# Optimization experiments

Measured on AMD Instinct MI355X. Metric: run time of the kernel, lower is better.

## Reference

```python
import jax, jax.numpy as jnp
import numpy as np

N_NODES = 50000
N_EDGES = 800000
D_FEAT = 64      # node feature dim -> edge input is 2*D_FEAT
HIDDEN = 128     # ebm hidden width (== 2*D_FEAT here)


def setup_inputs() -> dict:
    key = jax.random.key(0)
    ks = jax.random.split(key, 8)
    x = jax.random.normal(ks[0], (N_NODES, D_FEAT), dtype=jnp.float32)
    edge_index = jax.random.randint(ks[1], (2, N_EDGES), 0, N_NODES, dtype=jnp.int64)
    t = jax.random.uniform(ks[2], (N_EDGES,), dtype=jnp.float32)
    s1 = 1.0 / np.sqrt(2 * D_FEAT)
    s2 = 1.0 / np.sqrt(HIDDEN)
    W1 = jax.random.normal(ks[3], (2 * D_FEAT, HIDDEN), dtype=jnp.float32) * s1
    b1 = jnp.zeros((HIDDEN,), dtype=jnp.float32)
    Wt = jax.random.normal(ks[4], (1, HIDDEN), dtype=jnp.float32)
    bt = jnp.zeros((HIDDEN,), dtype=jnp.float32)
    W2 = jax.random.normal(ks[5], (HIDDEN, 2 * D_FEAT), dtype=jnp.float32) * s2
    b2 = jnp.zeros((2 * D_FEAT,), dtype=jnp.float32)
    return {"x": x, "edge_index": edge_index, "t": t,
            "W1": W1, "b1": b1, "Wt": Wt, "bt": bt, "W2": W2, "b2": b2}


def _ebm(edge_input, t, W1, b1, Wt, bt, W2, b2):
    # time-conditioned 2-layer SiLU MLP: [E, 2d] -> [E, 2d]
    t_emb = jax.nn.silu(t[:, None] * Wt + bt)            # [E, H]
    h = jax.nn.silu(edge_input @ W1 + t_emb + b1)        # [E, H]
    return h @ W2 + b2                                    # [E, 2d]


def reference(x, edge_index, t, W1, b1, Wt, bt, W2, b2):
    row, col = edge_index[0], edge_index[1]
    # gather endpoint features and concat -> [E, 2d]
    edge_input = jnp.concatenate([x[row], x[col]], axis=1)
    edge_output = _ebm(edge_input, t, W1, b1, Wt, bt, W2, b2)
    d = edge_output.shape[1] // 2
    src_update = edge_output[:, :d]
    tgt_update = edge_output[:, d:]
    update = jnp.concatenate([src_update, tgt_update], axis=0)  # [2E, d]
    idx = jnp.concatenate([row, col], axis=0)                   # [2E]
    # scatter_add into node slots
    return jax.ops.segment_sum(update, idx, num_segments=x.shape[0])
```

## Files before the change

kernel.cpp:

```cpp
#include <hip/hip_runtime.h>
#include <hip/hip_bf16.h>

#define NEDGE 800000
#define NNODE 50000
#define DF    64
#define HID   128
#define NTILE (NEDGE / 16)
#define BLK   768
#define WPB   12
#define TBINS 2048

using short8 = __attribute__((ext_vector_type(8))) short;
using f32x4  = __attribute__((ext_vector_type(4))) float;
using i32x4  = __attribute__((ext_vector_type(4))) int;

union P8 { unsigned int u[4]; short8 s; };

__device__ __forceinline__ unsigned int pk2(float lo, float hi) {
    union { __hip_bfloat162 p; unsigned int u; } c;
    c.p = __float22bfloat162_rn(float2{lo, hi});
    return c.u;
}

__device__ __forceinline__ unsigned short bf1(float f) {
    union { __hip_bfloat16 b; unsigned short u; } c;
    c.b = __float2bfloat16(f);
    return c.u;
}

__device__ __forceinline__ float bf2f(unsigned short u) {
    union { unsigned int i; float f; } c;
    c.i = ((unsigned int)u) << 16;
    return c.f;
}

__device__ __forceinline__ float exp2_hw(float x) {
    float r; asm("v_exp_f32 %0, %1" : "=v"(r) : "v"(x)); return r;
}
__device__ __forceinline__ float rcp_hw(float x) {
    float r; asm("v_rcp_f32 %0, %1" : "=v"(r) : "v"(x)); return r;
}
__device__ __forceinline__ float silu_f(float v) {
    return v * rcp_hw(1.0f + exp2_hw(v * -1.44269504f));
}

__device__ __forceinline__ short8 te_load(const unsigned short* __restrict__ ttbl,
                                          float tv, int jl) {
    const int tb = (int)(tv * (float)TBINS);
    return *(const short8*)(ttbl + (size_t)tb * HID + (jl << 3));
}

__device__ __forceinline__ int swz(int r, int k) {
    return (r << 8) + ((((k >> 3) ^ (r & 7)) << 4) | ((k & 7) << 1));
}
__device__ __forceinline__ int swz16(int r, int slot) {
    return (r << 8) + ((slot ^ (r & 7)) << 4);
}

__global__ void __launch_bounds__(256)
prep_kernel(const float* __restrict__ x, unsigned short* __restrict__ xb,
            const float* __restrict__ Wt, const float* __restrict__ bt,
            unsigned short* __restrict__ ttbl, int* __restrict__ counts)
{
    const int i = blockIdx.x * 256 + threadIdx.x;
    if (i < NNODE * DF / 8) {
        const f32x4 u = *(const f32x4*)(x + (size_t)i * 8);
        const f32x4 v = *(const f32x4*)(x + (size_t)i * 8 + 4);
        P8 p;
        p.u[0] = pk2(u[0], u[1]); p.u[1] = pk2(u[2], u[3]);
        p.u[2] = pk2(v[0], v[1]); p.u[3] = pk2(v[2], v[3]);
        *(short8*)(xb + (size_t)i * 8) = p.s;
    }
    if (i < TBINS * HID / 8) {
        const int bin = i >> 4;
        const int j0  = (i & 15) << 3;
        const float tv = (bin + 0.5f) * (1.0f / (float)TBINS);
        float e[8];
#pragma unroll
        for (int q = 0; q < 8; q++) e[q] = silu_f(fmaf(tv, Wt[j0 + q], bt[j0 + q]));
        P8 p;
        p.u[0] = pk2(e[0], e[1]); p.u[1] = pk2(e[2], e[3]);
        p.u[2] = pk2(e[4], e[5]); p.u[3] = pk2(e[6], e[7]);
        *(short8*)(ttbl + (size_t)bin * HID + j0) = p.s;
    }
    if (i < NNODE) counts[i] = 0;
}

__global__ void __launch_bounds__(256) hist_kernel(const int* __restrict__ ei,
                                                   int* __restrict__ counts) {
    const int i = blockIdx.x * 256 + threadIdx.x;
    if (i < 2 * NEDGE) atomicAdd(&counts[ei[i]], 1);
}

__global__ void __launch_bounds__(1024) scan1_kernel(const int* __restrict__ counts,
                                                     int* __restrict__ offs,
                                                     int* __restrict__ bsum) {
    __shared__ int buf[1024];
    const int tid = threadIdx.x;
    const int gid = blockIdx.x * 1024 + tid;
    const int v = (gid < NNODE) ? counts[gid] : 0;
    buf[tid] = v;
    __syncthreads();
#pragma unroll
    for (int off = 1; off < 1024; off <<= 1) {
        const int u = (tid >= off) ? buf[tid - off] : 0;
        __syncthreads();
        buf[tid] += u;
        __syncthreads();
    }
    if (gid < NNODE) offs[gid] = buf[tid] - v;
    if (tid == 1023) bsum[blockIdx.x] = buf[1023];
}

__global__ void __launch_bounds__(1024) scan2_kernel(int* __restrict__ bsum, int nb) {
    __shared__ int buf[1024];
    const int tid = threadIdx.x;
    const int v = (tid < nb) ? bsum[tid] : 0;
    buf[tid] = v;
    __syncthreads();
#pragma unroll
    for (int off = 1; off < 1024; off <<= 1) {
        const int u = (tid >= off) ? buf[tid - off] : 0;
        __syncthreads();
        buf[tid] += u;
        __syncthreads();
    }
    if (tid < nb) bsum[tid] = buf[tid] - v;
}

__global__ void __launch_bounds__(1024) scan3_kernel(int* __restrict__ offs,
                                                     const int* __restrict__ bsum,
                                                     int* __restrict__ cursor) {
    const int gid = blockIdx.x * 1024 + threadIdx.x;
    if (gid < NNODE) {
        const int o = offs[gid] + bsum[blockIdx.x];
        offs[gid] = o;
        cursor[gid] = o;
    }
    if (gid == 0) offs[NNODE] = 2 * NEDGE;
}

__global__ void __launch_bounds__(BLK, 3)
gnn_mlp_scatter(const unsigned short* __restrict__ xb, const int* __restrict__ ei,
                const float* __restrict__ t, const unsigned short* __restrict__ ttbl,
                const float* __restrict__ b1, const float* __restrict__ b2,
                const float* __restrict__ W1, const float* __restrict__ W2,
                unsigned short* __restrict__ eout, int* __restrict__ cursor)
{
    extern __shared__ char lds[];
    char* const w1s = lds;
    char* const w2s = lds + 32768;
    const int tid  = threadIdx.x;
    const int wave = tid >> 6;
    const int lane = tid & 63;
    char* const hs = lds + 65536 + (wave << 12);

    for (int idx = tid; idx < HID * HID; idx += BLK) {
        const int k = idx >> 7, j = idx & 127;
        const int rho = ((j & 7) << 4) + (j >> 3);
        *(unsigned short*)(w1s + swz(rho, k)) = bf1(W1[idx]);
        *(unsigned short*)(w2s + swz(rho, k)) = bf1(W2[idx]);
    }

    const int jl   = lane & 15;
    const int quad = lane >> 4;
    const int k0   = quad << 3;
    float b1j[8], b2j[8];
#pragma unroll
    for (int nt = 0; nt < 8; nt++) {
        const int j = jl * 8 + nt;
        b1j[nt] = b1[j]; b2j[nt] = b2[j];
    }
    __syncthreads();

    const int gwave = blockIdx.x * WPB + wave;
    const int nwave = gridDim.x * WPB;

#define ISSUE_EI(T, RA, CA) { const int e_ = (T) * 16 + jl; RA = ei[e_]; CA = ei[NEDGE + e_]; }
#define ISSUE_X(RA, CA, X_) { \
    const unsigned short* xr_ = xb + (RA) * DF + k0; \
    const unsigned short* xc_ = xb + (CA) * DF + k0; \
    X_[0] = *(const short8*)(xr_);      X_[1] = *(const short8*)(xr_ + 32); \
    X_[2] = *(const short8*)(xc_);      X_[3] = *(const short8*)(xc_ + 32); }
#define ISSUE_EP(T, T4_, RI_, CI_, TE_) { const int er_ = (T) * 16 + (quad << 2); \
    T4_ = *(const f32x4*)(t + er_); \
    RI_ = *(const i32x4*)(ei + er_); \
    CI_ = *(const i32x4*)(ei + NEDGE + er_); \
    TE_[0] = te_load(ttbl, T4_[0], jl); \
    TE_[1] = te_load(ttbl, T4_[1], jl); \
    TE_[2] = te_load(ttbl, T4_[2], jl); \
    TE_[3] = te_load(ttbl, T4_[3], jl); }

    int tile = gwave;
    if (tile < NTILE) {
        int riA, ciA;  ISSUE_EI(tile, riA, ciA);
        short8 X[4];   ISSUE_X(riA, ciA, X);
        f32x4 T4; i32x4 RI, CI; short8 TE[4]; ISSUE_EP(tile, T4, RI, CI, TE);
        int tn  = tile + nwave;
        int tns = (tn < NTILE) ? tn : gwave;
        int riA_n, ciA_n; ISSUE_EI(tns, riA_n, ciA_n);

        while (tile < NTILE) {
            short8 Xn[4]; ISSUE_X(riA_n, ciA_n, Xn);
            f32x4 T4n; i32x4 RIn, CIn; short8 TEn[4]; ISSUE_EP(tns, T4n, RIn, CIn, TEn);
            const int t2  = tn + nwave;
            const int t2s = (t2 < NTILE) ? t2 : gwave;
            int riA_nn, ciA_nn; ISSUE_EI(t2s, riA_nn, ciA_nn);

            int posS[4], posT[4];
            {
                unsigned int ps[4], pt[4];
#pragma unroll
                for (int r = 0; r < 4; r++) {
                    ps[r] = (jl == 0) ? atomicAdd((unsigned int*)&cursor[RI[r]], 1u) : 0u;
                    pt[r] = (jl == 8) ? atomicAdd((unsigned int*)&cursor[CI[r]], 1u) : 0u;
                }
#pragma unroll
                for (int r = 0; r < 4; r++) {
                    posS[r] = __shfl((int)ps[r], lane & 48);
                    posT[r] = __shfl((int)pt[r], (lane & 48) | 8);
                }
            }

            f32x4 acc1[8];
#pragma unroll
            for (int nt = 0; nt < 8; nt++) {
                f32x4 acc = {0.f, 0.f, 0.f, 0.f};
                const int rho = nt * 16 + jl;
#pragma unroll
                for (int kk = 0; kk < 4; kk++) {
                    const short8 bfr = *(const short8*)(w1s + swz16(rho, (kk << 2) + quad));
                    acc = __builtin_amdgcn_mfma_f32_16x16x32_bf16(X[kk], bfr, acc, 0, 0, 0);
                }
                acc1[nt] = acc;
            }

#pragma unroll
            for (int r = 0; r < 4; r++) {
                float h[8];
#pragma unroll
                for (int nt = 0; nt < 8; nt++) {
                    h[nt] = silu_f(acc1[nt][r] + bf2f((unsigned short)TE[r][nt]) + b1j[nt]);
                }
                P8 p;
                p.u[0] = pk2(h[0], h[1]);
                p.u[1] = pk2(h[2], h[3]);
                p.u[2] = pk2(h[4], h[5]);
                p.u[3] = pk2(h[6], h[7]);
                *(short8*)(hs + swz16((quad << 2) + r, jl)) = p.s;
            }

            short8 a2[4];
#pragma unroll
            for (int kk = 0; kk < 4; kk++) {
                a2[kk] = *(const short8*)(hs + swz16(jl, (kk << 2) + quad));
            }

            f32x4 acc2[8];
#pragma unroll
            for (int nt = 0; nt < 8; nt++) {
                f32x4 acc = {0.f, 0.f, 0.f, 0.f};
                const int rho = nt * 16 + jl;
#pragma unroll
                for (int kk = 0; kk < 4; kk++) {
                    const short8 bfr = *(const short8*)(w2s + swz16(rho, (kk << 2) + quad));
                    acc = __builtin_amdgcn_mfma_f32_16x16x32_bf16(a2[kk], bfr, acc, 0, 0, 0);
                }
                acc2[nt] = acc;
            }

#pragma unroll
            for (int r = 0; r < 4; r++) {
                const int pos = (jl < 8) ? posS[r] : posT[r];
                unsigned short* dst = eout + (size_t)pos * 64 + ((jl & 7) << 3);
                P8 p;
                p.u[0] = pk2(acc2[0][r] + b2j[0], acc2[1][r] + b2j[1]);
                p.u[1] = pk2(acc2[2][r] + b2j[2], acc2[3][r] + b2j[3]);
                p.u[2] = pk2(acc2[4][r] + b2j[4], acc2[5][r] + b2j[5]);
                p.u[3] = pk2(acc2[6][r] + b2j[6], acc2[7][r] + b2j[7]);
                *(short8*)dst = p.s;
            }

            tile = tn; tn = t2; tns = t2s;
#pragma unroll
            for (int i = 0; i < 4; i++) { X[i] = Xn[i]; TE[i] = TEn[i]; }
            T4 = T4n; RI = RIn; CI = CIn;
            riA_n = riA_nn; ciA_n = ciA_nn;
        }
    }
#undef ISSUE_EI
#undef ISSUE_X
#undef ISSUE_EP
}

__global__ void __launch_bounds__(256)
gather_kernel(const unsigned short* __restrict__ eout, const int* __restrict__ offs,
              float* __restrict__ out)
{
    const int grp = threadIdx.x >> 5;
    const int l32 = threadIdx.x & 31;
    const int n = blockIdx.x * 8 + grp;
    if (n >= NNODE) return;
    const int o0 = offs[n], o1 = offs[n + 1];

    const int cg = l32 & 7;
    const int rp = l32 >> 3;
    float acc[8] = {0.f, 0.f, 0.f, 0.f, 0.f, 0.f, 0.f, 0.f};
    for (int k = o0 + rp; k < o1; k += 4) {
        const short8 v = *(const short8*)(eout + (size_t)k * 64 + (cg << 3));
#pragma unroll
        for (int j = 0; j < 8; j++) acc[j] += bf2f((unsigned short)v[j]);
    }
#pragma unroll
    for (int j = 0; j < 8; j++) {
        acc[j] += __shfl_xor(acc[j], 8);
        acc[j] += __shfl_xor(acc[j], 16);
    }
    if (rp == 0) {
        float* o = out + (size_t)n * DF + (cg << 3);
        *(f32x4*)(o)     = f32x4{acc[0], acc[1], acc[2], acc[3]};
        *(f32x4*)(o + 4) = f32x4{acc[4], acc[5], acc[6], acc[7]};
    }
}

__global__ void __launch_bounds__(256, 2)
gnn_fused_atomic(const float* __restrict__ x, const int* __restrict__ ei,
                 const float* __restrict__ t,
                 const float* __restrict__ W1, const float* __restrict__ b1,
                 const float* __restrict__ Wt, const float* __restrict__ bt,
                 const float* __restrict__ W2, const float* __restrict__ b2,
                 float* __restrict__ out)
{
    extern __shared__ char lds[];
    char* const w1s = lds;
    char* const w2s = lds + 32768;
    const int tid  = threadIdx.x;
    const int wave = tid >> 6;
    const int lane = tid & 63;
    char* const hs = lds + 65536 + (wave << 12);

    for (int idx = tid; idx < HID * HID; idx += 256) {
        const int k = idx >> 7, j = idx & 127;
        const int off = swz(j, k);
        *(unsigned short*)(w1s + off) = bf1(W1[idx]);
        *(unsigned short*)(w2s + off) = bf1(W2[idx]);
    }

    const int jl   = lane & 15;
    const int quad = lane >> 4;
    const int k0   = quad << 3;
    float wtj[8], btj[8], b1j[8], b2j[8];
#pragma unroll
    for (int nt = 0; nt < 8; nt++) {
        const int j = nt * 16 + jl;
        wtj[nt] = Wt[j]; btj[nt] = bt[j]; b1j[nt] = b1[j]; b2j[nt] = b2[j];
    }
    __syncthreads();

    const int gwave = (blockIdx.x << 2) + wave;
    const int nwave = gridDim.x << 2;

    for (int tile = gwave; tile < NTILE; tile += nwave) {
        const int base = tile << 4;
        const int eA = base + jl;
        const int ri = ei[eA];
        const int ci = ei[NEDGE + eA];

        short8 a[4];
        {
            const float* xr_ = x + ri * DF + k0;
            const float* xc_ = x + ci * DF + k0;
            f32x4 u0 = *(const f32x4*)(xr_),      v0 = *(const f32x4*)(xr_ + 4);
            f32x4 u1 = *(const f32x4*)(xr_ + 32), v1 = *(const f32x4*)(xr_ + 36);
            f32x4 u2 = *(const f32x4*)(xc_),      v2 = *(const f32x4*)(xc_ + 4);
            f32x4 u3 = *(const f32x4*)(xc_ + 32), v3 = *(const f32x4*)(xc_ + 36);
            P8 p0, p1, p2, p3;
            p0.u[0]=pk2(u0[0],u0[1]); p0.u[1]=pk2(u0[2],u0[3]); p0.u[2]=pk2(v0[0],v0[1]); p0.u[3]=pk2(v0[2],v0[3]);
            p1.u[0]=pk2(u1[0],u1[1]); p1.u[1]=pk2(u1[2],u1[3]); p1.u[2]=pk2(v1[0],v1[1]); p1.u[3]=pk2(v1[2],v1[3]);
            p2.u[0]=pk2(u2[0],u2[1]); p2.u[1]=pk2(u2[2],u2[3]); p2.u[2]=pk2(v2[0],v2[1]); p2.u[3]=pk2(v2[2],v2[3]);
            p3.u[0]=pk2(u3[0],u3[1]); p3.u[1]=pk2(u3[2],u3[3]); p3.u[2]=pk2(v3[0],v3[1]); p3.u[3]=pk2(v3[2],v3[3]);
            a[0]=p0.s; a[1]=p1.s; a[2]=p2.s; a[3]=p3.s;
        }

        const int er = base + (quad << 2);
        const f32x4 T4 = *(const f32x4*)(t + er);
        const i32x4 RI = *(const i32x4*)(ei + er);
        const i32x4 CI = *(const i32x4*)(ei + NEDGE + er);

#pragma unroll
        for (int nt = 0; nt < 8; nt++) {
            f32x4 acc = {0.f, 0.f, 0.f, 0.f};
            const int j = nt * 16 + jl;
#pragma unroll
            for (int kk = 0; kk < 4; kk++) {
                const short8 bfr = *(const short8*)(w1s + swz16(j, (kk << 2) + quad));
                acc = __builtin_amdgcn_mfma_f32_16x16x32_bf16(a[kk], bfr, acc, 0, 0, 0);
            }
#pragma unroll
            for (int r = 0; r < 4; r++) {
                const float temb = silu_f(fmaf(T4[r], wtj[nt], btj[nt]));
                const float h = silu_f(acc[r] + temb + b1j[nt]);
                *(unsigned short*)(hs + swz((quad << 2) + r, j)) = bf1(h);
            }
        }

        short8 a2[4];
#pragma unroll
        for (int kk = 0; kk < 4; kk++) {
            a2[kk] = *(const short8*)(hs + swz16(jl, (kk << 2) + quad));
        }

#pragma unroll
        for (int nt = 0; nt < 8; nt++) {
            f32x4 acc = {0.f, 0.f, 0.f, 0.f};
            const int j = nt * 16 + jl;
#pragma unroll
            for (int kk = 0; kk < 4; kk++) {
                const short8 bfr = *(const short8*)(w2s + swz16(j, (kk << 2) + quad));
                acc = __builtin_amdgcn_mfma_f32_16x16x32_bf16(a2[kk], bfr, acc, 0, 0, 0);
            }
#pragma unroll
            for (int r = 0; r < 4; r++) {
                const float v = acc[r] + b2j[nt];
                const int node = (nt < 4) ? RI[r] : CI[r];
                unsafeAtomicAdd(out + node * DF + (j & 63), v);
            }
        }
    }
}

extern "C" void kernel_launch(void* const* d_in, const int* in_sizes, int n_in,
                              void* d_out, int out_size, void* d_ws, size_t ws_size,
                              hipStream_t stream) {
    const float* x  = (const float*)d_in[0];
    const int*   ei = (const int*)d_in[1];
    const float* t  = (const float*)d_in[2];
    const float* W1 = (const float*)d_in[3];
    const float* b1 = (const float*)d_in[4];
    const float* Wt = (const float*)d_in[5];
    const float* bt = (const float*)d_in[6];
    const float* W2 = (const float*)d_in[7];
    const float* b2 = (const float*)d_in[8];
    float* out = (float*)d_out;

    const size_t eoutB = (size_t)(2 * NEDGE) * 64 * sizeof(unsigned short);
    const size_t ttblB = (size_t)TBINS * HID * sizeof(unsigned short);
    const size_t need  = eoutB + ttblB + (size_t)(3 * NNODE + 1 + 1024) * sizeof(int) + 256;

    if (ws_size >= need) {
        char* wsb = (char*)d_ws;
        unsigned short* eout = (unsigned short*)wsb;
        unsigned short* ttbl = (unsigned short*)(wsb + eoutB);
        int* counts = (int*)(wsb + eoutB + ttblB);
        int* offs   = counts + NNODE;
        int* bsum   = offs + NNODE + 1;
        int* cursor = bsum + 1024;

        unsigned short* xb = (unsigned short*)d_out;

        const int nsb = (NNODE + 1023) / 1024;

        hipLaunchKernelGGL(prep_kernel, dim3((NNODE * DF / 8 + 255) / 256), dim3(256),
                           0, stream, x, xb, Wt, bt, ttbl, counts);
        hipLaunchKernelGGL(hist_kernel, dim3((2 * NEDGE + 255) / 256), dim3(256), 0, stream,
                           ei, counts);
        hipLaunchKernelGGL(scan1_kernel, dim3(nsb), dim3(1024), 0, stream,
                           counts, offs, bsum);
        hipLaunchKernelGGL(scan2_kernel, dim3(1), dim3(1024), 0, stream, bsum, nsb);
        hipLaunchKernelGGL(scan3_kernel, dim3(nsb), dim3(1024), 0, stream,
                           offs, bsum, cursor);

        const int ldsMlp = 65536 + WPB * 4096;
        (void)hipFuncSetAttribute((const void*)gnn_mlp_scatter,
                                  hipFuncAttributeMaxDynamicSharedMemorySize, ldsMlp);
        hipLaunchKernelGGL(gnn_mlp_scatter, dim3(256), dim3(BLK), ldsMlp, stream,
                           xb, ei, t, ttbl, b1, b2, W1, W2, eout, cursor);

        hipLaunchKernelGGL(gather_kernel, dim3((NNODE + 7) / 8), dim3(256), 0, stream,
                           eout, offs, out);
    } else {
        const int ldsBytes = 65536 + 4 * 4096;
        (void)hipMemsetAsync(out, 0, (size_t)out_size * sizeof(float), stream);
        (void)hipFuncSetAttribute((const void*)gnn_fused_atomic,
                                  hipFuncAttributeMaxDynamicSharedMemorySize, ldsBytes);
        hipLaunchKernelGGL(gnn_fused_atomic, dim3(512), dim3(256), ldsBytes, stream,
                           x, ei, t, W1, b1, Wt, bt, W2, b2, out);
    }
}
```

Baseline: 228.4 us.

## Process two 16-edge tiles per wave iteration, dropping cross-iteration prefetch

The main edge MLP kernel now handles 32 edges per loop iteration as two interleaved 16-row MFMA tiles, so each LDS weight fragment feeds two MFMAs. It drops the software-pipelined double buffering of gathered features and time embeddings and keeps only an index prefetch for the next tile. The time-embedding table lookups move after the first GEMM. This raises instruction-level parallelism and halves weight LDS reads per edge, at the cost of more registers and less latency hiding for the feature gathers.

```diff
diff --git a/kernel.cpp b/kernel.cpp
--- a/kernel.cpp
+++ b/kernel.cpp
@@ -5,7 +5,7 @@
 #define NNODE 50000
 #define DF    64
 #define HID   128
-#define NTILE (NEDGE / 16)
+#define NT32  (NEDGE / 32)
 #define BLK   768
 #define WPB   12
 #define TBINS 2048
@@ -176,121 +176,152 @@
     const int gwave = blockIdx.x * WPB + wave;
     const int nwave = gridDim.x * WPB;
 
-#define ISSUE_EI(T, RA, CA) { const int e_ = (T) * 16 + jl; RA = ei[e_]; CA = ei[NEDGE + e_]; }
-#define ISSUE_X(RA, CA, X_) { \
-    const unsigned short* xr_ = xb + (RA) * DF + k0; \
-    const unsigned short* xc_ = xb + (CA) * DF + k0; \
-    X_[0] = *(const short8*)(xr_);      X_[1] = *(const short8*)(xr_ + 32); \
-    X_[2] = *(const short8*)(xc_);      X_[3] = *(const short8*)(xc_ + 32); }
-#define ISSUE_EP(T, T4_, RI_, CI_, TE_) { const int er_ = (T) * 16 + (quad << 2); \
-    T4_ = *(const f32x4*)(t + er_); \
-    RI_ = *(const i32x4*)(ei + er_); \
-    CI_ = *(const i32x4*)(ei + NEDGE + er_); \
-    TE_[0] = te_load(ttbl, T4_[0], jl); \
-    TE_[1] = te_load(ttbl, T4_[1], jl); \
-    TE_[2] = te_load(ttbl, T4_[2], jl); \
-    TE_[3] = te_load(ttbl, T4_[3], jl); }
-
     int tile = gwave;
-    if (tile < NTILE) {
-        int riA, ciA;  ISSUE_EI(tile, riA, ciA);
-        short8 X[4];   ISSUE_X(riA, ciA, X);
-        f32x4 T4; i32x4 RI, CI; short8 TE[4]; ISSUE_EP(tile, T4, RI, CI, TE);
-        int tn  = tile + nwave;
-        int tns = (tn < NTILE) ? tn : gwave;
-        int riA_n, ciA_n; ISSUE_EI(tns, riA_n, ciA_n);
-
-        while (tile < NTILE) {
-            short8 Xn[4]; ISSUE_X(riA_n, ciA_n, Xn);
-            f32x4 T4n; i32x4 RIn, CIn; short8 TEn[4]; ISSUE_EP(tns, T4n, RIn, CIn, TEn);
-            const int t2  = tn + nwave;
-            const int t2s = (t2 < NTILE) ? t2 : gwave;
-            int riA_nn, ciA_nn; ISSUE_EI(t2s, riA_nn, ciA_nn);
-
-            int posS[4], posT[4];
+    if (tile < NT32) {
+        int rA, cA, rB, cB;
+        {
+            const int e0 = tile * 32 + jl;
+            rA = ei[e0]; cA = ei[NEDGE + e0];
+            rB = ei[e0 + 16]; cB = ei[NEDGE + e0 + 16];
+        }
+
+        while (tile < NT32) {
+            short8 X0[4], X1[4];
             {
-                unsigned int ps[4], pt[4];
-#pragma unroll
-                for (int r = 0; r < 4; r++) {
-                    ps[r] = (jl == 0) ? atomicAdd((unsigned int*)&cursor[RI[r]], 1u) : 0u;
-                    pt[r] = (jl == 8) ? atomicAdd((unsigned int*)&cursor[CI[r]], 1u) : 0u;
-                }
-#pragma unroll
-                for (int r = 0; r < 4; r++) {
-                    posS[r] = __shfl((int)ps[r], lane & 48);
-                    posT[r] = __shfl((int)pt[r], (lane & 48) | 8);
-                }
-            }
-
-            f32x4 acc1[8];
+                const unsigned short* xr = xb + rA * DF + k0;
+                const unsigned short* xc = xb + cA * DF + k0;
+                X0[0] = *(const short8*)(xr); X0[1] = *(const short8*)(xr + 32);
+                X0[2] = *(const short8*)(xc); X0[3] = *(const short8*)(xc + 32);
+                const unsigned short* yr = xb + rB * DF + k0;
+                const unsigned short* yc = xb + cB * DF + k0;
+                X1[0] = *(const short8*)(yr); X1[1] = *(const short8*)(yr + 32);
+                X1[2] = *(const short8*)(yc); X1[3] = *(const short8*)(yc + 32);
+            }
+            const int er0 = tile * 32 + (quad << 2);
+            const f32x4 T40 = *(const f32x4*)(t + er0);
+            const i32x4 RI0 = *(const i32x4*)(ei + er0);
+            const i32x4 CI0 = *(const i32x4*)(ei + NEDGE + er0);
+            const f32x4 T41 = *(const f32x4*)(t + er0 + 16);
+            const i32x4 RI1 = *(const i32x4*)(ei + er0 + 16);
+            const i32x4 CI1 = *(const i32x4*)(ei + NEDGE + er0 + 16);
+
+            const int tn  = tile + nwave;
+            const int tns = (tn < NT32) ? tn : gwave;
+            int rA_n, cA_n, rB_n, cB_n;
+            {
+                const int e0 = tns * 32 + jl;
+                rA_n = ei[e0]; cA_n = ei[NEDGE + e0];
+                rB_n = ei[e0 + 16]; cB_n = ei[NEDGE + e0 + 16];
+            }
+
+            unsigned int ps0[4], pt0[4], ps1[4], pt1[4];
+#pragma unroll
+            for (int r = 0; r < 4; r++) {
+                ps0[r] = (jl == 0) ? atomicAdd((unsigned int*)&cursor[RI0[r]], 1u) : 0u;
+                pt0[r] = (jl == 8) ? atomicAdd((unsigned int*)&cursor[CI0[r]], 1u) : 0u;
+                ps1[r] = (jl == 0) ? atomicAdd((unsigned int*)&cursor[RI1[r]], 1u) : 0u;
+                pt1[r] = (jl == 8) ? atomicAdd((unsigned int*)&cursor[CI1[r]], 1u) : 0u;
+            }
+
+            f32x4 acc1A[8], acc1B[8];
 #pragma unroll
             for (int nt = 0; nt < 8; nt++) {
-                f32x4 acc = {0.f, 0.f, 0.f, 0.f};
+                f32x4 aA = {0.f, 0.f, 0.f, 0.f};
+                f32x4 aB = {0.f, 0.f, 0.f, 0.f};
                 const int rho = nt * 16 + jl;
 #pragma unroll
                 for (int kk = 0; kk < 4; kk++) {
                     const short8 bfr = *(const short8*)(w1s + swz16(rho, (kk << 2) + quad));
-                    acc = __builtin_amdgcn_mfma_f32_16x16x32_bf16(X[kk], bfr, acc, 0, 0, 0);
+                    aA = __builtin_amdgcn_mfma_f32_16x16x32_bf16(X0[kk], bfr, aA, 0, 0, 0);
+                    aB = __builtin_amdgcn_mfma_f32_16x16x32_bf16(X1[kk], bfr, aB, 0, 0, 0);
                 }
-                acc1[nt] = acc;
-            }
-
+                acc1A[nt] = aA; acc1B[nt] = aB;
+            }
+
+            short8 TE0[4], TE1[4];
+#pragma unroll
+            for (int r = 0; r < 4; r++) {
+                TE0[r] = te_load(ttbl, T40[r], jl);
+                TE1[r] = te_load(ttbl, T41[r], jl);
+            }
+
+            short8 a2A[4], a2B[4];
 #pragma unroll
             for (int r = 0; r < 4; r++) {
                 float h[8];
 #pragma unroll
-                for (int nt = 0; nt < 8; nt++) {
-                    h[nt] = silu_f(acc1[nt][r] + bf2f((unsigned short)TE[r][nt]) + b1j[nt]);
-                }
+                for (int nt = 0; nt < 8; nt++)
+                    h[nt] = silu_f(acc1A[nt][r] + bf2f((unsigned short)TE0[r][nt]) + b1j[nt]);
                 P8 p;
-                p.u[0] = pk2(h[0], h[1]);
-                p.u[1] = pk2(h[2], h[3]);
-                p.u[2] = pk2(h[4], h[5]);
-                p.u[3] = pk2(h[6], h[7]);
+                p.u[0] = pk2(h[0], h[1]); p.u[1] = pk2(h[2], h[3]);
+                p.u[2] = pk2(h[4], h[5]); p.u[3] = pk2(h[6], h[7]);
                 *(short8*)(hs + swz16((quad << 2) + r, jl)) = p.s;
             }
-
-            short8 a2[4];
-#pragma unroll
-            for (int kk = 0; kk < 4; kk++) {
-                a2[kk] = *(const short8*)(hs + swz16(jl, (kk << 2) + quad));
-            }
-
-            f32x4 acc2[8];
+#pragma unroll
+            for (int kk = 0; kk < 4; kk++)
+                a2A[kk] = *(const short8*)(hs + swz16(jl, (kk << 2) + quad));
+
+#pragma unroll
+            for (int r = 0; r < 4; r++) {
+                float h[8];
+#pragma unroll
+                for (int nt = 0; nt < 8; nt++)
+                    h[nt] = silu_f(acc1B[nt][r] + bf2f((unsigned short)TE1[r][nt]) + b1j[nt]);
+                P8 p;
+                p.u[0] = pk2(h[0], h[1]); p.u[1] = pk2(h[2], h[3]);
+                p.u[2] = pk2(h[4], h[5]); p.u[3] = pk2(h[6], h[7]);
+                *(short8*)(hs + swz16((quad << 2) + r, jl)) = p.s;
+            }
+#pragma unroll
+            for (int kk = 0; kk < 4; kk++)
+                a2B[kk] = *(const short8*)(hs + swz16(jl, (kk << 2) + quad));
+
+            f32x4 acc2A[8], acc2B[8];
 #pragma unroll
             for (int nt = 0; nt < 8; nt++) {
-                f32x4 acc = {0.f, 0.f, 0.f, 0.f};
+                f32x4 aA = {0.f, 0.f, 0.f, 0.f};
+                f32x4 aB = {0.f, 0.f, 0.f, 0.f};
                 const int rho = nt * 16 + jl;
 #pragma unroll
                 for (int kk = 0; kk < 4; kk++) {
                     const short8 bfr = *(const short8*)(w2s + swz16(rho, (kk << 2) + quad));
-                    acc = __builtin_amdgcn_mfma_f32_16x16x32_bf16(a2[kk], bfr, acc, 0, 0, 0);
+                    aA = __builtin_amdgcn_mfma_f32_16x16x32_bf16(a2A[kk], bfr, aA, 0, 0, 0);
+                    aB = __builtin_amdgcn_mfma_f32_16x16x32_bf16(a2B[kk], bfr, aB, 0, 0, 0);
                 }
-                acc2[nt] = acc;
-            }
-
-#pragma unroll
-            for (int r = 0; r < 4; r++) {
-                const int pos = (jl < 8) ? posS[r] : posT[r];
+                acc2A[nt] = aA; acc2B[nt] = aB;
+            }
+
+#pragma unroll
+            for (int r = 0; r < 4; r++) {
+                const int posS = __shfl((int)ps0[r], lane & 48);
+                const int posT = __shfl((int)pt0[r], (lane & 48) | 8);
+                const int pos  = (jl < 8) ? posS : posT;
                 unsigned short* dst = eout + (size_t)pos * 64 + ((jl & 7) << 3);
                 P8 p;
-                p.u[0] = pk2(acc2[0][r] + b2j[0], acc2[1][r] + b2j[1]);
-                p.u[1] = pk2(acc2[2][r] + b2j[2], acc2[3][r] + b2j[3]);
-                p.u[2] = pk2(acc2[4][r] + b2j[4], acc2[5][r] + b2j[5]);
-                p.u[3] = pk2(acc2[6][r] + b2j[6], acc2[7][r] + b2j[7]);
+                p.u[0] = pk2(acc2A[0][r] + b2j[0], acc2A[1][r] + b2j[1]);
+                p.u[1] = pk2(acc2A[2][r] + b2j[2], acc2A[3][r] + b2j[3]);
+                p.u[2] = pk2(acc2A[4][r] + b2j[4], acc2A[5][r] + b2j[5]);
+                p.u[3] = pk2(acc2A[6][r] + b2j[6], acc2A[7][r] + b2j[7]);
                 *(short8*)dst = p.s;
             }
-
-            tile = tn; tn = t2; tns = t2s;
-#pragma unroll
-            for (int i = 0; i < 4; i++) { X[i] = Xn[i]; TE[i] = TEn[i]; }
-            T4 = T4n; RI = RIn; CI = CIn;
-            riA_n = riA_nn; ciA_n = ciA_nn;
+#pragma unroll
+            for (int r = 0; r < 4; r++) {
+                const int posS = __shfl((int)ps1[r], lane & 48);
+                const int posT = __shfl((int)pt1[r], (lane & 48) | 8);
+                const int pos  = (jl < 8) ? posS : posT;
+                unsigned short* dst = eout + (size_t)pos * 64 + ((jl & 7) << 3);
+                P8 p;
+                p.u[0] = pk2(acc2B[0][r] + b2j[0], acc2B[1][r] + b2j[1]);
+                p.u[1] = pk2(acc2B[2][r] + b2j[2], acc2B[3][r] + b2j[3]);
+                p.u[2] = pk2(acc2B[4][r] + b2j[4], acc2B[5][r] + b2j[5]);
+                p.u[3] = pk2(acc2B[6][r] + b2j[6], acc2B[7][r] + b2j[7]);
+                *(short8*)dst = p.s;
+            }
+
+            rA = rA_n; cA = cA_n; rB = rB_n; cB = cB_n;
+            tile = tn;
         }
     }
-#undef ISSUE_EI
-#undef ISSUE_X
-#undef ISSUE_EP
 }
 
 __global__ void __launch_bounds__(256)
@@ -360,7 +391,7 @@
     const int gwave = (blockIdx.x << 2) + wave;
     const int nwave = gridDim.x << 2;
 
-    for (int tile = gwave; tile < NTILE; tile += nwave) {
+    for (int tile = gwave; tile < NEDGE / 16; tile += nwave) {
         const int base = tile << 4;
         const int eA = base + jl;
         const int ri = ei[eA];
```

After: 292.3 us. +28.0%, slower.
